# Kernel tuning notes

Hardware: AMD Instinct MI355X
Metric: run time of the kernel (lower is better)

Reference implementation:

```python
import jax, jax.numpy as jnp
import numpy as np

VOCAB = 32000
D = 256        # embedding dim
NB = 256       # n_bubbles
NEQ = 5        # n_equilibrium_steps
THRESH = 1.5   # surprise_threshold
SEQ = 64
DECAYS = np.array([0.3, 0.7, 0.9], dtype=np.float32)  # RunningKnow frame decay rates


def setup_inputs() -> dict:
    key = jax.random.key(0)
    k1, k2, k3 = jax.random.split(key, 3)
    tokens = jax.random.randint(k1, (SEQ,), 0, VOCAB)
    E = jax.random.normal(k2, (VOCAB, D), dtype=jnp.float32)
    # Foam bubble measurement operators (stand-in: per-bubble linear map), scaled for sane stats
    W = jax.random.normal(k3, (NB, D, D), dtype=jnp.float32) / np.float32(np.sqrt(D))
    return {
        "tokens": tokens,
        "E": E,
        "W": W,
        "memory_decay_base": jnp.asarray(0.8, dtype=jnp.float32),
        "novelty_sensitivity": jnp.asarray(1.0, dtype=jnp.float32),
    }


def _equilibrate(m):
    # Stand-in for Foam.equilibrate: NEQ relaxation steps toward the bubble mean.
    for _ in range(NEQ):
        m = m + 0.1 * (m.mean(axis=0, keepdims=True) - m)
    return m


def reference(tokens, E, W, memory_decay_base, novelty_sensitivity):
    dr = jnp.asarray(DECAYS)[:, None, None]          # [F,1,1]
    F = dr.shape[0]
    sens = jnp.abs(novelty_sensitivity)

    def step(carry, tok):
        memory, means, vars_, n_seen = carry
        x = E[tok]                                   # [D]
        mm = memory.mean(axis=0)                     # [D]
        mem_norm = jnp.linalg.norm(mm) + 1e-10
        x_norm = jnp.linalg.norm(x) + 1e-10
        novelty = jnp.where(mem_norm > 1e-8,
                            1.0 - jnp.dot(x, mm) / (x_norm * mem_norm),
                            jnp.float32(1.0))
        decay = jax.nn.sigmoid(memory_decay_base - sens * novelty)
        xm = x + decay * mm                          # [D]

        meas = jnp.einsum('d,nde->ne', xm, W)        # [NB,D] bubble measurements

        # RunningKnow.evaluate (blank model at n_seen==0 -> never knows)
        std = jnp.sqrt(vars_ + 1e-8)                 # [F,NB,D]
        surprise = (jnp.abs(meas[None] - means) / std).mean(axis=(1, 2))  # [F]
        any_knows = jnp.any((surprise < THRESH) & (n_seen > 0))

        eq = _equilibrate(meas)
        eff = jnp.where(any_knows, meas, eq)         # know -> skip equilibration
        eff_d = jax.lax.stop_gradient(eff)           # .detach() in torch

        # RunningKnow.update (EMA mean/var per frame; first call initializes)
        upd_mean = dr * means + (1.0 - dr) * eff_d
        upd_var = jnp.maximum(dr * vars_ + (1.0 - dr) * (eff_d - means) * (eff_d - upd_mean), 1e-8)
        first = (n_seen == 0)
        means = jnp.where(first, jnp.broadcast_to(eff_d, (F, NB, D)), upd_mean)
        vars_ = jnp.where(first, jnp.float32(0.1), upd_var)

        # density matrix and spectrum
        mnorm = eff / (jnp.linalg.norm(eff, axis=-1, keepdims=True) + 1e-10)  # [NB,D]
        rho = mnorm.T @ mnorm / NB                   # [D,D]
        eigs = jnp.linalg.eigvalsh(jax.lax.stop_gradient(rho))
        eigs = jnp.maximum(eigs, 1e-12)
        eigs = eigs / eigs.sum()

        memory = decay * memory + (1.0 - decay) * eff_d
        logits = ((E @ rho) * E).sum(axis=-1)        # [VOCAB]
        return (memory, means, vars_, n_seen + 1), (logits, eigs)

    carry0 = (jnp.zeros((NB, D), jnp.float32),
              jnp.zeros((F, NB, D), jnp.float32),
              jnp.ones((F, NB, D), jnp.float32),
              jnp.int32(0))
    _, (logits, eigs) = jax.lax.scan(step, carry0, tokens)
    return logits, eigs  # [SEQ,VOCAB], [SEQ,D]
```

## Files before the change

### kernel.cpp

```cpp
#include <hip/hip_runtime.h>
#include <hip/hip_bf16.h>
#include <cstdint>
#include <cstddef>

constexpr size_t OFF_MEM    = 0;
constexpr size_t OFF_XM     = 65536;
constexpr size_t OFF_MU     = 82176;
constexpr size_t OFF_SABS   = 98560;
constexpr size_t OFF_BAR    = 98816;
constexpr size_t ZERO_END   = 98880;
constexpr size_t OFF_WBAR   = 98880;
constexpr size_t OFF_MEANS  = 164416;
constexpr size_t OFF_VARS   = 361024;
constexpr size_t OFF_DT     = 557632;
constexpr size_t OFF_ET     = 574016;
constexpr size_t OFF_RHO    = 590400;
constexpr size_t OFF_MN16   = 4784704;
constexpr size_t OFF_E16    = 6881856;
constexpr size_t WS_FLOATS  = 10977856;

#define SEQ_ 64
#define VOCAB_ 32000

typedef __attribute__((ext_vector_type(8))) short bf16x8;
typedef __attribute__((ext_vector_type(4))) float f32x4;

__device__ __forceinline__ float wave_sum(float v){
  v += __shfl_xor(v, 32); v += __shfl_xor(v, 16); v += __shfl_xor(v, 8);
  v += __shfl_xor(v, 4);  v += __shfl_xor(v, 2);  v += __shfl_xor(v, 1);
  return v;
}
__device__ __forceinline__ float block_sum(float v, float* red){
  int tid = threadIdx.x;
  v = wave_sum(v);
  if ((tid & 63) == 0) red[tid >> 6] = v;
  __syncthreads();
  float r = red[0] + red[1] + red[2] + red[3];
  __syncthreads();
  return r;
}
__device__ __forceinline__ float block_min(float v, float* red){
  int tid = threadIdx.x;
  v = fminf(v, __shfl_xor(v, 32)); v = fminf(v, __shfl_xor(v, 16));
  v = fminf(v, __shfl_xor(v, 8));  v = fminf(v, __shfl_xor(v, 4));
  v = fminf(v, __shfl_xor(v, 2));  v = fminf(v, __shfl_xor(v, 1));
  if ((tid & 63) == 0) red[tid >> 6] = v;
  __syncthreads();
  float r = fminf(fminf(red[0], red[1]), fminf(red[2], red[3]));
  __syncthreads();
  return r;
}
__device__ __forceinline__ float block_max(float v, float* red){
  int tid = threadIdx.x;
  v = fmaxf(v, __shfl_xor(v, 32)); v = fmaxf(v, __shfl_xor(v, 16));
  v = fmaxf(v, __shfl_xor(v, 8));  v = fmaxf(v, __shfl_xor(v, 4));
  v = fmaxf(v, __shfl_xor(v, 2));  v = fmaxf(v, __shfl_xor(v, 1));
  if ((tid & 63) == 0) red[tid >> 6] = v;
  __syncthreads();
  float r = fmaxf(fmaxf(red[0], red[1]), fmaxf(red[2], red[3]));
  __syncthreads();
  return r;
}

__global__ __launch_bounds__(256) void k0_init(const float* __restrict__ E, float* __restrict__ ws){
  size_t i = (size_t)blockIdx.x * 256 + threadIdx.x;
  if (i < ZERO_END) ws[i] = 0.f;
  __hip_bfloat16* e16 = (__hip_bfloat16*)(ws + OFF_E16);
  e16[i] = __float2bfloat16(E[i]);
}

__global__ __launch_bounds__(256) void k_wbar(const float* __restrict__ W, float* __restrict__ ws){
  size_t i = (size_t)blockIdx.x * 256 + threadIdx.x;
  float s = 0.f;
  #pragma unroll 4
  for (int n = 0; n < 256; ++n)
    s += W[(size_t)n * 65536 + i];
  ws[OFF_WBAR + i] = s * (1.0f / 256.0f);
}

__global__ __launch_bounds__(1024) void k_xm(const int* __restrict__ tokens,
    const float* __restrict__ E, const float* __restrict__ mdbp,
    const float* __restrict__ nsp, float* __restrict__ ws){
  __shared__ float xm_s[256];
  __shared__ __align__(16) float part[4][256];
  __shared__ float redA[16], redB[16], redC[16];
  const int tid = threadIdx.x;
  const int e = tid & 255, q = tid >> 8;
  const int lane = tid & 63, w = tid >> 6;
  const float sens = fabsf(nsp[0]);
  const float mdb  = mdbp[0];
  const float* Wb = ws + OFF_WBAR;
  float mm = 0.f;

  for (int t = 0; t < SEQ_; ++t){
    int tok = tokens[t];
    float xv = (tid < 256) ? E[(size_t)tok * 256 + e] : 0.f;
    float a = wave_sum(xv * mm);
    float b = wave_sum(xv * xv);
    float c = wave_sum(mm * mm);
    if (lane == 0){ redA[w] = a; redB[w] = b; redC[w] = c; }
    __syncthreads();
    float sdot = (redA[0] + redA[1]) + (redA[2] + redA[3]);
    float sx2  = (redB[0] + redB[1]) + (redB[2] + redB[3]);
    float sm2  = (redC[0] + redC[1]) + (redC[2] + redC[3]);
    float mem_norm = sqrtf(sm2) + 1e-10f;
    float x_norm   = sqrtf(sx2) + 1e-10f;
    float novelty = (mem_norm > 1e-8f) ? (1.0f - sdot / (x_norm * mem_norm)) : 1.0f;
    float z = mdb - sens * novelty;
    float decay = 1.0f / (1.0f + expf(-z));
    if (tid < 256){
      float xmv = xv + decay * mm;
      xm_s[e] = xmv;
      ws[OFF_XM + (size_t)e * 64 + t] = xmv;
    }
    __syncthreads();

    const float* Wq = Wb + (size_t)(q * 64) * 256 + e;
    float p = 0.f;
    #pragma unroll 16
    for (int dd = 0; dd < 64; ++dd)
      p = fmaf(xm_s[q * 64 + dd], Wq[(size_t)dd * 256], p);
    part[q][e] = p;
    __syncthreads();
    if (tid < 256){
      float acc = (part[0][e] + part[1][e]) + (part[2][e] + part[3][e]);
      ws[OFF_MU + (size_t)t * 256 + e] = acc;
      mm = decay * mm + (1.0f - decay) * acc;
    }
    __syncthreads();
  }
}

__global__ __launch_bounds__(256) void k_measall(const float* __restrict__ W, float* __restrict__ ws){
  __shared__ __align__(16) float xm_s[16384];
  const int tid = threadIdx.x, n = blockIdx.x;
  for (int i = tid; i < 16384; i += 256) xm_s[i] = ws[OFF_XM + i];
  __syncthreads();

  float acc[64];
  #pragma unroll
  for (int t = 0; t < 64; ++t) acc[t] = 0.f;

  const float* Wn = W + (size_t)n * 65536 + tid;
  for (int d = 0; d < 256; ++d){
    float wv = Wn[(size_t)d * 256];
    const float* xr = &xm_s[d * 64];
    #pragma unroll
    for (int q = 0; q < 16; ++q){
      float4 x4 = *(const float4*)&xr[q * 4];
      acc[q * 4 + 0] = fmaf(x4.x, wv, acc[q * 4 + 0]);
      acc[q * 4 + 1] = fmaf(x4.y, wv, acc[q * 4 + 1]);
      acc[q * 4 + 2] = fmaf(x4.z, wv, acc[q * 4 + 2]);
      acc[q * 4 + 3] = fmaf(x4.w, wv, acc[q * 4 + 3]);
    }
  }
  #pragma unroll
  for (int t = 0; t < 64; ++t)
    ws[OFF_RHO + (size_t)n * 16384 + (size_t)t * 256 + tid] = acc[t];
}

__global__ __launch_bounds__(1024, 1) void k_stats(float* __restrict__ ws){
  __shared__ float redA[16], redB[16], redC[16];
  const int tid = threadIdx.x;
  const int e = tid & 255, q = tid >> 8;
  const int lane = tid & 63, w = tid >> 6;
  const int n = blockIdx.x * 4 + q;
  unsigned* bar = (unsigned*)(ws + OFF_BAR);
  __hip_bfloat16* mn16 = (__hip_bfloat16*)(ws + OFF_MN16);
  const size_t ne = (size_t)n * 256 + e;
  const float TH = 1.5f * 65536.0f;
  const float c5 = 0.59049f;

  float mean0 = 0.f, mean1 = 0.f, mean2 = 0.f;
  float var0 = 0.f, var1 = 0.f, var2 = 0.f;

  for (int t = 0; t < SEQ_; ++t){
    float me = ws[OFF_RHO + (size_t)n * 16384 + (size_t)t * 256 + e];
    bool know = false;
    if (t > 0){
      float v0 = fabsf(me - mean0) / sqrtf(var0 + 1e-8f);
      float v1 = fabsf(me - mean1) / sqrtf(var1 + 1e-8f);
      float v2 = fabsf(me - mean2) / sqrtf(var2 + 1e-8f);
      float a = wave_sum(v0), b = wave_sum(v1), c = wave_sum(v2);
      if (lane == 0){ redA[w] = a; redB[w] = b; redC[w] = c; }
      __syncthreads();
      if (tid == 0){
        float sA = 0.f, sB = 0.f, sC = 0.f;
        #pragma unroll
        for (int i = 0; i < 16; ++i){ sA += redA[i]; sB += redB[i]; sC += redC[i]; }
        atomicAdd(&ws[OFF_SABS + (size_t)t * 4 + 0], sA);
        atomicAdd(&ws[OFF_SABS + (size_t)t * 4 + 1], sB);
        atomicAdd(&ws[OFF_SABS + (size_t)t * 4 + 2], sC);
        __hip_atomic_fetch_add(bar, 1u, __ATOMIC_ACQ_REL, __HIP_MEMORY_SCOPE_AGENT);
        unsigned tgt = 64u * (unsigned)t;
        while (__hip_atomic_load(bar, __ATOMIC_ACQUIRE, __HIP_MEMORY_SCOPE_AGENT) < tgt)
          __builtin_amdgcn_s_sleep(2);
      }
      __syncthreads();
      float s0 = __hip_atomic_load(&ws[OFF_SABS + (size_t)t * 4 + 0], __ATOMIC_RELAXED, __HIP_MEMORY_SCOPE_AGENT);
      float s1 = __hip_atomic_load(&ws[OFF_SABS + (size_t)t * 4 + 1], __ATOMIC_RELAXED, __HIP_MEMORY_SCOPE_AGENT);
      float s2 = __hip_atomic_load(&ws[OFF_SABS + (size_t)t * 4 + 2], __ATOMIC_RELAXED, __HIP_MEMORY_SCOPE_AGENT);
      know = (s0 < TH) || (s1 < TH) || (s2 < TH);
    }
    float mu = ws[OFF_MU + (size_t)t * 256 + e];
    float eq = c5 * me + (1.0f - c5) * mu;
    float eff = know ? me : eq;

    if (t == 0){
      mean0 = eff; mean1 = eff; mean2 = eff;
      var0 = 0.1f; var1 = 0.1f; var2 = 0.1f;
    } else {
      float um, uv;
      um = 0.3f * mean0 + 0.7f * eff;
      uv = 0.3f * var0 + 0.7f * (eff - mean0) * (eff - um);
      mean0 = um; var0 = fmaxf(uv, 1e-8f);
      um = 0.7f * mean1 + 0.3f * eff;
      uv = 0.7f * var1 + 0.3f * (eff - mean1) * (eff - um);
      mean1 = um; var1 = fmaxf(uv, 1e-8f);
      um = 0.9f * mean2 + 0.1f * eff;
      uv = 0.9f * var2 + 0.1f * (eff - mean2) * (eff - um);
      mean2 = um; var2 = fmaxf(uv, 1e-8f);
    }

    float nv = wave_sum(eff * eff);
    if (lane == 0) redA[w] = nv;
    __syncthreads();
    float nr2 = (redA[4 * q + 0] + redA[4 * q + 1]) + (redA[4 * q + 2] + redA[4 * q + 3]);
    float rn = sqrtf(nr2) + 1e-10f;
    mn16[(size_t)t * 65536 + ne] = __float2bfloat16(eff / rn);
    __syncthreads();
  }
}

__global__ __launch_bounds__(256) void k_rho(float* __restrict__ ws){
  const int t = blockIdx.x, rb = blockIdx.y, tid = threadIdx.x;
  __shared__ __align__(16) float tile[32][256];
  const __hip_bfloat16* mn16 = (const __hip_bfloat16*)(ws + OFF_MN16);
  float acc[32];
  #pragma unroll
  for (int i = 0; i < 32; ++i) acc[i] = 0.f;
  for (int c = 0; c < 8; ++c){
    __syncthreads();
    for (int j = tid; j < 8192; j += 256){
      int row = j >> 8, col = j & 255;
      tile[row][col] = __bfloat162float(mn16[(size_t)t * 65536 + (size_t)(c * 32 + row) * 256 + col]);
    }
    __syncthreads();
    for (int nl = 0; nl < 32; ++nl){
      float ev = tile[nl][tid];
      #pragma unroll
      for (int q = 0; q < 8; ++q){
        float4 dv = *(const float4*)&tile[nl][rb * 32 + q * 4];
        acc[q * 4 + 0] = fmaf(dv.x, ev, acc[q * 4 + 0]);
        acc[q * 4 + 1] = fmaf(dv.y, ev, acc[q * 4 + 1]);
        acc[q * 4 + 2] = fmaf(dv.z, ev, acc[q * 4 + 2]);
        acc[q * 4 + 3] = fmaf(dv.w, ev, acc[q * 4 + 3]);
      }
    }
  }
  #pragma unroll
  for (int i = 0; i < 32; ++i)
    ws[OFF_RHO + (size_t)t * 65536 + (size_t)(rb * 32 + i) * 256 + tid] = acc[i] * (1.0f / 256.0f);
}

__global__ __launch_bounds__(512, 2) void k_trigemm(float* __restrict__ ws, float* __restrict__ out){
  __shared__ __align__(16) char smem_raw[51200];
  const int tid = threadIdx.x;

  if (blockIdx.x < 64){
    float* ca   = (float*)smem_raw;
    float* ua   = ca + 256;
    float* wa   = ua + 256;
    float* ph   = wa + 256;
    float* redA = ph + 512;
    float* redB = redA + 8;
    const int t = blockIdx.x;
    const int c = tid & 255, h = tid >> 8;
    const float* rho = ws + OFF_RHO + (size_t)t * 65536;
    float* dT = ws + OFF_DT + (size_t)t * 256;
    float* eT = ws + OFF_ET + (size_t)t * 256;

    float Mreg[128];
    {
      const float* Mc = rho + (size_t)(h * 128) * 256 + c;
      #pragma unroll
      for (int rr = 0; rr < 128; ++rr)
        Mreg[rr] = Mc[(size_t)rr * 256];
    }
    const int rowbase = h * 128;

    for (int k = 0; k < 254; ++k){
      __syncthreads();
      if (c == k){
        #pragma unroll
        for (int rr = 0; rr < 128; ++rr) ca[rowbase + rr] = Mreg[rr];
      }
      __syncthreads();
      float uval = 0.f;
      if (tid < 256){
        float raw = ca[tid];
        uval = (tid > k) ? raw : 0.f;
        ua[tid] = uval;
        if (tid == 0) dT[k] = ca[k];
      }
      float pa = wave_sum(uval * uval);
      if ((tid & 63) == 0) redA[tid >> 6] = pa;
      __syncthreads();
      float sigma2 = redA[0] + redA[1] + redA[2] + redA[3]
                   + redA[4] + redA[5] + redA[6] + redA[7];
      float v0 = ca[k + 1];
      if (sigma2 < 1e-30f){
        if (tid == 0) eT[k] = v0;
        continue;
      }
      float sig = sqrtf(sigma2);
      float alpha = (v0 >= 0.f) ? -sig : sig;
      float u0 = v0 - alpha;
      float beta = 2.0f / (sigma2 - v0 * v0 + u0 * u0);
      if (tid == 0) eT[k] = alpha;
      if (tid == k + 1) ua[tid] = u0;
      __syncthreads();

      {
        float a0 = 0.f, a1 = 0.f, a2 = 0.f, a3 = 0.f;
        #pragma unroll
        for (int rr = 0; rr < 128; rr += 4){
          float4 u4 = *(const float4*)&ua[rowbase + rr];
          a0 = fmaf(Mreg[rr + 0], u4.x, a0);
          a1 = fmaf(Mreg[rr + 1], u4.y, a1);
          a2 = fmaf(Mreg[rr + 2], u4.z, a2);
          a3 = fmaf(Mreg[rr + 3], u4.w, a3);
        }
        ph[tid] = (a0 + a1) + (a2 + a3);
      }
      __syncthreads();
      float p = ph[c] + ph[c + 256];
      float up = (tid < 256) ? ua[tid] * p : 0.f;
      float pb = wave_sum(up);
      if ((tid & 63) == 0) redB[tid >> 6] = pb;
      __syncthreads();
      float s = redB[0] + redB[1] + redB[2] + redB[3]
              + redB[4] + redB[5] + redB[6] + redB[7];
      if (tid < 256) wa[tid] = (tid > k) ? (beta * p - 0.5f * beta * beta * s * ua[tid]) : 0.f;
      __syncthreads();
      {
        float ucv = ua[c], wcv = wa[c];
        #pragma unroll
        for (int rr = 0; rr < 128; rr += 4){
          float4 u4 = *(const float4*)&ua[rowbase + rr];
          float4 w4 = *(const float4*)&wa[rowbase + rr];
          Mreg[rr + 0] = fmaf(-w4.x, ucv, fmaf(-u4.x, wcv, Mreg[rr + 0]));
          Mreg[rr + 1] = fmaf(-w4.y, ucv, fmaf(-u4.y, wcv, Mreg[rr + 1]));
          Mreg[rr + 2] = fmaf(-w4.z, ucv, fmaf(-u4.z, wcv, Mreg[rr + 2]));
          Mreg[rr + 3] = fmaf(-w4.w, ucv, fmaf(-u4.w, wcv, Mreg[rr + 3]));
        }
      }
    }

    __syncthreads();
    if (c == 254){
      #pragma unroll
      for (int rr = 0; rr < 128; ++rr) ca[rowbase + rr] = Mreg[rr];
    }
    __syncthreads();
    if (tid == 0){ dT[254] = ca[254]; eT[254] = ca[255]; }
    __syncthreads();
    if (c == 255){
      #pragma unroll
      for (int rr = 0; rr < 128; ++rr) ca[rowbase + rr] = Mreg[rr];
    }
    __syncthreads();
    if (tid == 0){ dT[255] = ca[255]; eT[255] = 0.f; }
  } else {
    short* A_lds = (short*)smem_raw;
    short* B_lds = A_lds + 8192;
    float* pl    = (float*)(B_lds + 16384);
    const int g = blockIdx.x - 64;
    const int bx = g % 250, t = g / 250;
    const int lane = tid & 63, w = tid >> 6;
    const int wr = w >> 2, wc = w & 3;
    const int vbase = bx * 128;
    const short* E16 = (const short*)(ws + OFF_E16);
    const short* MN  = (const short*)(ws + OFF_MN16) + (size_t)t * 65536;

    f32x4 acc[4][4];
    #pragma unroll
    for (int i = 0; i < 4; ++i)
      #pragma unroll
      for (int j = 0; j < 4; ++j){ f32x4 z = {0.f, 0.f, 0.f, 0.f}; acc[i][j] = z; }

    const int gq = lane >> 4, r16 = lane & 15;
    const int sx = r16 & 7;
    for (int it = 0; it < 4; ++it){
      const int k0 = it * 64;
      __syncthreads();
      #pragma unroll
      for (int pa = 0; pa < 2; ++pa){
        int ch = pa * 512 + tid;
        int row = ch >> 3, c8 = ch & 7;
        int sc8 = c8 ^ (row & 7);
        uint4 v = *(const uint4*)(E16 + (size_t)(vbase + row) * 256 + k0 + sc8 * 8);
        *(uint4*)&A_lds[ch * 8] = v;
      }
      #pragma unroll
      for (int pb = 0; pb < 4; ++pb){
        int ch = pb * 512 + tid;
        int row = ch >> 3, c8 = ch & 7;
        int sc8 = c8 ^ (row & 7);
        uint4 v = *(const uint4*)(MN + (size_t)row * 256 + k0 + sc8 * 8);
        *(uint4*)&B_lds[ch * 8] = v;
      }
      __syncthreads();
      #pragma unroll
      for (int kk = 0; kk < 64; kk += 32){
        const int j0 = (kk >> 3) + gq;
        bf16x8 af[4], bf[4];
        #pragma unroll
        for (int fm = 0; fm < 4; ++fm)
          af[fm] = *(const bf16x8*)&A_lds[(wr * 64 + fm * 16 + r16) * 64 + (j0 ^ sx) * 8];
        #pragma unroll
        for (int fn = 0; fn < 4; ++fn)
          bf[fn] = *(const bf16x8*)&B_lds[(wc * 64 + fn * 16 + r16) * 64 + (j0 ^ sx) * 8];
        #pragma unroll
        for (int fm = 0; fm < 4; ++fm)
          #pragma unroll
          for (int fn = 0; fn < 4; ++fn)
            acc[fm][fn] = __builtin_amdgcn_mfma_f32_16x16x32_bf16(af[fm], bf[fn], acc[fm][fn], 0, 0, 0);
      }
    }

    float ps[4][4];
    #pragma unroll
    for (int fm = 0; fm < 4; ++fm)
      #pragma unroll
      for (int i = 0; i < 4; ++i){
        float sv = 0.f;
        #pragma unroll
        for (int fn = 0; fn < 4; ++fn){ float v = acc[fm][fn][i]; sv += v * v; }
        sv += __shfl_xor(sv, 1); sv += __shfl_xor(sv, 2);
        sv += __shfl_xor(sv, 4); sv += __shfl_xor(sv, 8);
        ps[fm][i] = sv;
      }
    __syncthreads();
    if (r16 == 0){
      #pragma unroll
      for (int fm = 0; fm < 4; ++fm)
        #pragma unroll
        for (int i = 0; i < 4; ++i)
          pl[w * 64 + fm * 16 + gq * 4 + i] = ps[fm][i];
    }
    __syncthreads();
    if (tid < 128){
      int rr = tid;
      int wrr = rr >> 6, lr = rr & 63;
      float sum = pl[(wrr * 4 + 0) * 64 + lr] + pl[(wrr * 4 + 1) * 64 + lr]
                + pl[(wrr * 4 + 2) * 64 + lr] + pl[(wrr * 4 + 3) * 64 + lr];
      out[(size_t)t * VOCAB_ + vbase + rr] = sum * (1.0f / 256.0f);
    }
  }
}

__global__ __launch_bounds__(256) void k_bisect(const float* __restrict__ ws, float* __restrict__ out){
  __shared__ float d_s[256];
  __shared__ float e2_s[256];
  __shared__ float ea_s[256];
  __shared__ float red[4];
  const int t = blockIdx.x, tid = threadIdx.x;
  d_s[tid] = ws[OFF_DT + (size_t)t * 256 + tid];
  float evv = (tid < 255) ? ws[OFF_ET + (size_t)t * 256 + tid] : 0.f;
  e2_s[tid] = evv * evv;
  ea_s[tid] = fabsf(evv);
  __syncthreads();
  float rad = ea_s[tid] + ((tid > 0) ? ea_s[tid - 1] : 0.f);
  float glo = block_min(d_s[tid] - rad, red);
  float ghi = block_max(d_s[tid] + rad, red);

  float l = glo, h = ghi;
  for (int it = 0; it < 40; ++it){
    float mid = 0.5f * (l + h);
    float q = d_s[0] - mid;
    int cnt = (q < 0.f) ? 1 : 0;
    #pragma unroll 8
    for (int i = 1; i < 256; ++i){
      float qr = __builtin_amdgcn_rcpf(q);
      q = (d_s[i] - mid) - e2_s[i - 1] * qr;
      q = (fabsf(q) < 1e-25f) ? -1e-25f : q;
      cnt += (q < 0.f) ? 1 : 0;
    }
    if (cnt <= tid) l = mid; else h = mid;
  }
  float lam = fmaxf(0.5f * (l + h), 1e-12f);
  float ssum = block_sum(lam, red);
  out[(size_t)SEQ_ * VOCAB_ + (size_t)t * 256 + tid] = lam / ssum;
}

extern "C" void kernel_launch(void* const* d_in, const int* in_sizes, int n_in,
                              void* d_out, int out_size, void* d_ws, size_t ws_size,
                              hipStream_t stream){
  const int*   tokens = (const int*)d_in[0];
  const float* E      = (const float*)d_in[1];
  const float* W      = (const float*)d_in[2];
  const float* mdbp   = (const float*)d_in[3];
  const float* nsp    = (const float*)d_in[4];
  float* out = (float*)d_out;
  float* ws  = (float*)d_ws;
  if (ws_size < WS_FLOATS * sizeof(float)) return;

  k0_init<<<dim3(32000), dim3(256), 0, stream>>>(E, ws);
  k_wbar<<<dim3(256), dim3(256), 0, stream>>>(W, ws);
  k_xm<<<dim3(1), dim3(1024), 0, stream>>>(tokens, E, mdbp, nsp, ws);
  k_measall<<<dim3(256), dim3(256), 0, stream>>>(W, ws);
  {
    void* args[1];
    args[0] = (void*)&ws;
    hipLaunchCooperativeKernel((const void*)k_stats, dim3(64), dim3(1024), args, 0, stream);
  }
  k_rho<<<dim3(64, 8), dim3(256), 0, stream>>>(ws);
  k_trigemm<<<dim3(64 + 250 * 64), dim3(512), 0, stream>>>(ws, out);
  k_bisect<<<dim3(64), dim3(256), 0, stream>>>(ws, out);
}
```

Before: 3.182 ms.

## Fuse bisection into tridiagonalization blocks, cache Wbar in registers, vectorize rho loads

```diff
diff --git a/kernel.cpp b/kernel.cpp
--- a/kernel.cpp
+++ b/kernel.cpp
@@ -39,28 +39,6 @@
   __syncthreads();
   return r;
 }
-__device__ __forceinline__ float block_min(float v, float* red){
-  int tid = threadIdx.x;
-  v = fminf(v, __shfl_xor(v, 32)); v = fminf(v, __shfl_xor(v, 16));
-  v = fminf(v, __shfl_xor(v, 8));  v = fminf(v, __shfl_xor(v, 4));
-  v = fminf(v, __shfl_xor(v, 2));  v = fminf(v, __shfl_xor(v, 1));
-  if ((tid & 63) == 0) red[tid >> 6] = v;
-  __syncthreads();
-  float r = fminf(fminf(red[0], red[1]), fminf(red[2], red[3]));
-  __syncthreads();
-  return r;
-}
-__device__ __forceinline__ float block_max(float v, float* red){
-  int tid = threadIdx.x;
-  v = fmaxf(v, __shfl_xor(v, 32)); v = fmaxf(v, __shfl_xor(v, 16));
-  v = fmaxf(v, __shfl_xor(v, 8));  v = fmaxf(v, __shfl_xor(v, 4));
-  v = fmaxf(v, __shfl_xor(v, 2));  v = fmaxf(v, __shfl_xor(v, 1));
-  if ((tid & 63) == 0) red[tid >> 6] = v;
-  __syncthreads();
-  float r = fmaxf(fmaxf(red[0], red[1]), fmaxf(red[2], red[3]));
-  __syncthreads();
-  return r;
-}
 
 __global__ __launch_bounds__(256) void k0_init(const float* __restrict__ E, float* __restrict__ ws){
   size_t i = (size_t)blockIdx.x * 256 + threadIdx.x;
@@ -78,7 +56,7 @@
   ws[OFF_WBAR + i] = s * (1.0f / 256.0f);
 }
 
-__global__ __launch_bounds__(1024) void k_xm(const int* __restrict__ tokens,
+__global__ __launch_bounds__(1024, 1) void k_xm(const int* __restrict__ tokens,
     const float* __restrict__ E, const float* __restrict__ mdbp,
     const float* __restrict__ nsp, float* __restrict__ ws){
   __shared__ float xm_s[256];
@@ -92,6 +70,14 @@
   const float* Wb = ws + OFF_WBAR;
   float mm = 0.f;
 
+  float wreg[64];
+  {
+    const float* Wq = Wb + (size_t)(q * 64) * 256 + e;
+    #pragma unroll
+    for (int dd = 0; dd < 64; ++dd)
+      wreg[dd] = Wq[(size_t)dd * 256];
+  }
+
   for (int t = 0; t < SEQ_; ++t){
     int tok = tokens[t];
     float xv = (tid < 256) ? E[(size_t)tok * 256 + e] : 0.f;
@@ -115,11 +101,10 @@
     }
     __syncthreads();
 
-    const float* Wq = Wb + (size_t)(q * 64) * 256 + e;
     float p = 0.f;
-    #pragma unroll 16
+    #pragma unroll
     for (int dd = 0; dd < 64; ++dd)
-      p = fmaf(xm_s[q * 64 + dd], Wq[(size_t)dd * 256], p);
+      p = fmaf(xm_s[q * 64 + dd], wreg[dd], p);
     part[q][e] = p;
     __syncthreads();
     if (tid < 256){
@@ -235,15 +220,24 @@
 __global__ __launch_bounds__(256) void k_rho(float* __restrict__ ws){
   const int t = blockIdx.x, rb = blockIdx.y, tid = threadIdx.x;
   __shared__ __align__(16) float tile[32][256];
-  const __hip_bfloat16* mn16 = (const __hip_bfloat16*)(ws + OFF_MN16);
+  const unsigned short* mn16 = (const unsigned short*)(ws + OFF_MN16);
   float acc[32];
   #pragma unroll
   for (int i = 0; i < 32; ++i) acc[i] = 0.f;
   for (int c = 0; c < 8; ++c){
     __syncthreads();
-    for (int j = tid; j < 8192; j += 256){
-      int row = j >> 8, col = j & 255;
-      tile[row][col] = __bfloat162float(mn16[(size_t)t * 65536 + (size_t)(c * 32 + row) * 256 + col]);
+    #pragma unroll
+    for (int v = 0; v < 4; ++v){
+      int idx = v * 256 + tid;
+      int row = idx >> 5, c16 = idx & 31;
+      uint4 u4 = *(const uint4*)(mn16 + (size_t)t * 65536 + (size_t)(c * 32 + row) * 256 + c16 * 8);
+      float* dst = &tile[row][c16 * 8];
+      unsigned uu[4] = {u4.x, u4.y, u4.z, u4.w};
+      #pragma unroll
+      for (int j = 0; j < 4; ++j){
+        dst[j * 2 + 0] = __uint_as_float(uu[j] << 16);
+        dst[j * 2 + 1] = __uint_as_float(uu[j] & 0xffff0000u);
+      }
     }
     __syncthreads();
     for (int nl = 0; nl < 32; ++nl){
@@ -274,11 +268,12 @@
     float* ph   = wa + 256;
     float* redA = ph + 512;
     float* redB = redA + 8;
+    float* dd   = redB + 8;
+    float* ee   = dd + 256;
     const int t = blockIdx.x;
     const int c = tid & 255, h = tid >> 8;
+    const int lane = tid & 63, w = tid >> 6;
     const float* rho = ws + OFF_RHO + (size_t)t * 65536;
-    float* dT = ws + OFF_DT + (size_t)t * 256;
-    float* eT = ws + OFF_ET + (size_t)t * 256;
 
     float Mreg[128];
     {
@@ -301,7 +296,7 @@
         float raw = ca[tid];
         uval = (tid > k) ? raw : 0.f;
         ua[tid] = uval;
-        if (tid == 0) dT[k] = ca[k];
+        if (tid == 0) dd[k] = ca[k];
       }
       float pa = wave_sum(uval * uval);
       if ((tid & 63) == 0) redA[tid >> 6] = pa;
@@ -310,14 +305,14 @@
                    + redA[4] + redA[5] + redA[6] + redA[7];
       float v0 = ca[k + 1];
       if (sigma2 < 1e-30f){
-        if (tid == 0) eT[k] = v0;
+        if (tid == 0) ee[k] = v0;
         continue;
       }
       float sig = sqrtf(sigma2);
       float alpha = (v0 >= 0.f) ? -sig : sig;
       float u0 = v0 - alpha;
       float beta = 2.0f / (sigma2 - v0 * v0 + u0 * u0);
-      if (tid == 0) eT[k] = alpha;
+      if (tid == 0) ee[k] = alpha;
       if (tid == k + 1) ua[tid] = u0;
       __syncthreads();
 
@@ -363,14 +358,59 @@
       for (int rr = 0; rr < 128; ++rr) ca[rowbase + rr] = Mreg[rr];
     }
     __syncthreads();
-    if (tid == 0){ dT[254] = ca[254]; eT[254] = ca[255]; }
+    if (tid == 0){ dd[254] = ca[254]; ee[254] = ca[255]; }
     __syncthreads();
     if (c == 255){
       #pragma unroll
       for (int rr = 0; rr < 128; ++rr) ca[rowbase + rr] = Mreg[rr];
     }
     __syncthreads();
-    if (tid == 0){ dT[255] = ca[255]; eT[255] = 0.f; }
+    if (tid == 0){ dd[255] = ca[255]; ee[255] = 0.f; }
+    __syncthreads();
+
+    float dvv = dd[c];
+    float evv = ee[c];
+    if (h == 0){ ua[c] = evv * evv; ph[c] = fabsf(evv); }
+    __syncthreads();
+    float rad = ph[c] + ((c > 0) ? ph[c - 1] : 0.f);
+    float vmin = dvv - rad, vmax = dvv + rad;
+    vmin = fminf(vmin, __shfl_xor(vmin, 32)); vmin = fminf(vmin, __shfl_xor(vmin, 16));
+    vmin = fminf(vmin, __shfl_xor(vmin, 8));  vmin = fminf(vmin, __shfl_xor(vmin, 4));
+    vmin = fminf(vmin, __shfl_xor(vmin, 2));  vmin = fminf(vmin, __shfl_xor(vmin, 1));
+    vmax = fmaxf(vmax, __shfl_xor(vmax, 32)); vmax = fmaxf(vmax, __shfl_xor(vmax, 16));
+    vmax = fmaxf(vmax, __shfl_xor(vmax, 8));  vmax = fmaxf(vmax, __shfl_xor(vmax, 4));
+    vmax = fmaxf(vmax, __shfl_xor(vmax, 2));  vmax = fmaxf(vmax, __shfl_xor(vmax, 1));
+    if (lane == 0){ redA[w] = vmin; redB[w] = vmax; }
+    __syncthreads();
+    float glo = fminf(fminf(fminf(redA[0], redA[1]), fminf(redA[2], redA[3])),
+                      fminf(fminf(redA[4], redA[5]), fminf(redA[6], redA[7])));
+    float ghi = fmaxf(fmaxf(fmaxf(redB[0], redB[1]), fmaxf(redB[2], redB[3])),
+                      fmaxf(fmaxf(redB[4], redB[5]), fmaxf(redB[6], redB[7])));
+    __syncthreads();
+
+    float lo = glo, hi = ghi;
+    for (int it = 0; it < 40; ++it){
+      float mid = 0.5f * (lo + hi);
+      float qv = dd[0] - mid;
+      int cnt = (qv < 0.f) ? 1 : 0;
+      #pragma unroll 8
+      for (int i = 1; i < 256; ++i){
+        float qr = __builtin_amdgcn_rcpf(qv);
+        qv = (dd[i] - mid) - ua[i - 1] * qr;
+        qv = (fabsf(qv) < 1e-25f) ? -1e-25f : qv;
+        cnt += (qv < 0.f) ? 1 : 0;
+      }
+      if (cnt <= c) lo = mid; else hi = mid;
+    }
+    float lam = fmaxf(0.5f * (lo + hi), 1e-12f);
+    float lp = (h == 0) ? lam : 0.f;
+    lp = wave_sum(lp);
+    if (lane == 0) redA[w] = lp;
+    __syncthreads();
+    float ssum = ((redA[0] + redA[1]) + (redA[2] + redA[3]))
+               + ((redA[4] + redA[5]) + (redA[6] + redA[7]));
+    if (h == 0)
+      out[(size_t)SEQ_ * VOCAB_ + (size_t)t * 256 + c] = lam / ssum;
   } else {
     short* A_lds = (short*)smem_raw;
     short* B_lds = A_lds + 8192;
@@ -460,40 +500,6 @@
   }
 }
 
-__global__ __launch_bounds__(256) void k_bisect(const float* __restrict__ ws, float* __restrict__ out){
-  __shared__ float d_s[256];
-  __shared__ float e2_s[256];
-  __shared__ float ea_s[256];
-  __shared__ float red[4];
-  const int t = blockIdx.x, tid = threadIdx.x;
-  d_s[tid] = ws[OFF_DT + (size_t)t * 256 + tid];
-  float evv = (tid < 255) ? ws[OFF_ET + (size_t)t * 256 + tid] : 0.f;
-  e2_s[tid] = evv * evv;
-  ea_s[tid] = fabsf(evv);
-  __syncthreads();
-  float rad = ea_s[tid] + ((tid > 0) ? ea_s[tid - 1] : 0.f);
-  float glo = block_min(d_s[tid] - rad, red);
-  float ghi = block_max(d_s[tid] + rad, red);
-
-  float l = glo, h = ghi;
-  for (int it = 0; it < 40; ++it){
-    float mid = 0.5f * (l + h);
-    float q = d_s[0] - mid;
-    int cnt = (q < 0.f) ? 1 : 0;
-    #pragma unroll 8
-    for (int i = 1; i < 256; ++i){
-      float qr = __builtin_amdgcn_rcpf(q);
-      q = (d_s[i] - mid) - e2_s[i - 1] * qr;
-      q = (fabsf(q) < 1e-25f) ? -1e-25f : q;
-      cnt += (q < 0.f) ? 1 : 0;
-    }
-    if (cnt <= tid) l = mid; else h = mid;
-  }
-  float lam = fmaxf(0.5f * (l + h), 1e-12f);
-  float ssum = block_sum(lam, red);
-  out[(size_t)SEQ_ * VOCAB_ + (size_t)t * 256 + tid] = lam / ssum;
-}
-
 extern "C" void kernel_launch(void* const* d_in, const int* in_sizes, int n_in,
                               void* d_out, int out_size, void* d_ws, size_t ws_size,
                               hipStream_t stream){
@@ -517,5 +523,4 @@
   }
   k_rho<<<dim3(64, 8), dim3(256), 0, stream>>>(ws);
   k_trigemm<<<dim3(64 + 250 * 64), dim3(512), 0, stream>>>(ws, out);
-  k_bisect<<<dim3(64), dim3(256), 0, stream>>>(ws, out);
-}
+}
```

Result: faster. 3.104 ms (-2.4%).
